# Performance work log

Measured on AMD Instinct MI355X. Metric: run time of the kernel, lower is better.

## Reference

```python
import jax, jax.numpy as jnp
import numpy as np

D_IN = 1024
D_OUT = 1024
NUM_HEADS = 16
HEAD_DIM = D_OUT // NUM_HEADS
SEQ = 2048
BATCH = 2


def setup_inputs() -> dict:
    key = jax.random.key(0)
    k1, k2, k3 = jax.random.split(key, 3)
    x = jax.random.normal(k1, (BATCH, SEQ, D_IN), dtype=jnp.float32)
    w_qkv = jax.random.normal(k2, (3 * D_OUT, D_IN), dtype=jnp.float32) * (1.0 / np.sqrt(D_IN))
    w_proj = jax.random.normal(k3, (D_OUT, D_OUT), dtype=jnp.float32) * (1.0 / np.sqrt(D_OUT))
    b_proj = jnp.zeros((D_OUT,), dtype=jnp.float32)
    return {"x": x, "w_qkv": w_qkv, "w_proj": w_proj, "b_proj": b_proj}


def reference(x, w_qkv, w_proj, b_proj):
    B, S, _ = x.shape
    # QKV projection (no bias, qkv_bias=False)
    qkv = x @ w_qkv.T                              # [B,S,3*D]
    qkv = qkv.reshape(B, S, 3, NUM_HEADS, HEAD_DIM)
    q = qkv[:, :, 0].transpose(0, 2, 1, 3)          # [B,H,S,hd]
    k = qkv[:, :, 1].transpose(0, 2, 1, 3)
    v = qkv[:, :, 2].transpose(0, 2, 1, 3)
    scores = jnp.einsum('bhqd,bhkd->bhqk', q, k)    # [B,H,S,S]
    causal = jnp.triu(jnp.ones((S, S), dtype=bool), k=1)
    scores = jnp.where(causal, -jnp.inf, scores)
    weights = jax.nn.softmax(scores / np.sqrt(HEAD_DIM), axis=-1)
    ctx = jnp.einsum('bhqk,bhkd->bhqd', weights, v)  # [B,H,S,hd]
    ctx = ctx.transpose(0, 2, 1, 3).reshape(B, S, D_OUT)
    return ctx @ w_proj.T + b_proj
```

## Files before the change

kernel.cpp:

```cpp
#include <hip/hip_runtime.h>
#include <hip/hip_bf16.h>
#include <stdint.h>

#define NHEAD 16
#define HDIM  64
#define SEQ   2048
#define BATCH 2

typedef __attribute__((ext_vector_type(8))) short          s16x8;
typedef __attribute__((ext_vector_type(4))) short          s16x4;
typedef __attribute__((ext_vector_type(4))) float          f32x4;
typedef __attribute__((ext_vector_type(8))) unsigned short u16x8;
typedef __attribute__((ext_vector_type(4))) unsigned short u16x4;

__device__ __forceinline__ unsigned short f2b(float f) {
  union { float f; unsigned u; } x; x.f = f;
  unsigned r = x.u + 0x7fffu + ((x.u >> 16) & 1u);
  return (unsigned short)(r >> 16);
}
__device__ __forceinline__ float b2f(unsigned short b) {
  union { unsigned u; float f; } x; x.u = ((unsigned)b) << 16;
  return x.f;
}

__device__ __forceinline__ void gload_lds16(const void* g, void* l) {
  __builtin_amdgcn_global_load_lds((const __attribute__((address_space(1))) void*)g,
                                   (__attribute__((address_space(3))) void*)l,
                                   16, 0, 0);
}

#define SWZ(a) ((a) ^ ((((a) >> 7) & 7) << 4))

__global__ __launch_bounds__(256) void cvt3(
    const float* __restrict__ a, unsigned short* __restrict__ oa, int na,
    const float* __restrict__ b, unsigned short* __restrict__ ob, int nb,
    const float* __restrict__ c, unsigned short* __restrict__ oc) {
  int idx = (blockIdx.x * 256 + threadIdx.x) * 4;
  const float* in; unsigned short* out;
  if (idx < na)            { in = a; out = oa; }
  else if (idx < na + nb)  { in = b; out = ob; idx -= na; }
  else                     { in = c; out = oc; idx -= na + nb; }
  float4 v = *(const float4*)(in + idx);
  u16x4 o;
  o[0] = f2b(v.x); o[1] = f2b(v.y); o[2] = f2b(v.z); o[3] = f2b(v.w);
  *(u16x4*)(out + idx) = o;
}

template <int EPI, int M, int N, int K>
__global__ __launch_bounds__(256) void gemm_bt(
    const unsigned short* __restrict__ A,
    const unsigned short* __restrict__ B,
    unsigned short* __restrict__ oq,
    unsigned short* __restrict__ ok,
    unsigned short* __restrict__ ov,
    float* __restrict__ out,
    const float* __restrict__ bias) {
  __shared__ unsigned short As[128 * 64];
  __shared__ unsigned short Bs[128 * 64];

  constexpr int mtiles = M >> 7, ntiles = N >> 7;
  constexpr int mpx = mtiles >> 2, npx = ntiles >> 1;
  const int xcd = blockIdx.x & 7, j = blockIdx.x >> 3;
  const int mb = (xcd >> 1) * mpx + (j % mpx);
  const int nb = (xcd & 1) * npx + (j / mpx);
  const int mbase = mb << 7, nbase = nb << 7;

  const int tid  = threadIdx.x;
  const int lane = tid & 63;
  const int wid  = tid >> 6;
  const int wr   = (wid >> 1) * 64;
  const int wc   = (wid & 1) * 64;

  f32x4 acc[4][4];
  for (int r = 0; r < 4; ++r)
    for (int c = 0; c < 4; ++c) acc[r][c] = (f32x4){0.f, 0.f, 0.f, 0.f};

  const int rowA = lane >> 3;
  const int kbs  = ((lane & 7) * 16) ^ (rowA << 4);
  const size_t strideA = (size_t)K * 2;

  for (int kt = 0; kt < K; kt += 64) {
    for (int it = 0; it < 4; ++it) {
      int c   = wid * 4 + it;
      int row = c * 8 + rowA;
      gload_lds16((const char*)A + (size_t)(mbase + row) * strideA + (size_t)kt * 2 + kbs,
                  (char*)As + c * 1024 + (lane & 7) * 16);
      gload_lds16((const char*)B + (size_t)(nbase + row) * strideA + (size_t)kt * 2 + kbs,
                  (char*)Bs + c * 1024 + (lane & 7) * 16);
    }
    __syncthreads();
    const int sw = (lane & 7) << 4;
    for (int ks = 0; ks < 2; ++ks) {
      const int colb = ks * 64 + (lane >> 4) * 16;
      s16x8 af[4], bf[4];
      for (int r = 0; r < 4; ++r)
        af[r] = *(const s16x8*)((const char*)As + (wr + r * 16 + (lane & 15)) * 128 + (colb ^ sw));
      for (int c = 0; c < 4; ++c)
        bf[c] = *(const s16x8*)((const char*)Bs + (wc + c * 16 + (lane & 15)) * 128 + (colb ^ sw));
      for (int r = 0; r < 4; ++r)
        for (int c = 0; c < 4; ++c)
          acc[r][c] = __builtin_amdgcn_mfma_f32_16x16x32_bf16(af[r], bf[c], acc[r][c], 0, 0, 0);
    }
    __syncthreads();
  }

  for (int r = 0; r < 4; ++r) {
    for (int c = 0; c < 4; ++c) {
      const int n = nbase + wc + c * 16 + (lane & 15);
      for (int i = 0; i < 4; ++i) {
        const int m = mbase + wr + r * 16 + (lane >> 4) * 4 + i;
        float v = acc[r][c][i];
        if (EPI == 0) {
          int b = m >> 11, s = m & (SEQ - 1);
          int which = n >> 10, rr = n & 1023;
          int h = rr >> 6, d = rr & (HDIM - 1);
          if (which == 0)
            oq[(((size_t)b * NHEAD + h) * SEQ + s) * HDIM + d] = f2b(v);
          else if (which == 1)
            ok[(((size_t)b * NHEAD + h) * SEQ + s) * HDIM + d] = f2b(v);
          else
            ov[(((size_t)b * NHEAD + h) * HDIM + d) * SEQ + s] = f2b(v);
        } else {
          out[(size_t)m * N + n] = v + bias[n];
        }
      }
    }
  }
}

__global__ __launch_bounds__(256, 4) void flash_attn(
    const unsigned short* __restrict__ Qb,
    const unsigned short* __restrict__ Kb,
    const unsigned short* __restrict__ Vb,
    unsigned short* __restrict__ ctx) {
  const int bsw  = (int)blockIdx.x;
  const int lin  = ((bsw & 7) << 6) + (bsw >> 3);
  const int bh   = lin >> 4;
  const int pair = lin & 15;
  const int b    = bh >> 4;
  const int h    = bh & (NHEAD - 1);

  const unsigned short* Qh  = Qb + (size_t)bh * SEQ * HDIM;
  const char*           Khc = (const char*)(Kb + (size_t)bh * SEQ * HDIM);
  const char*           Vtc = (const char*)(Vb + (size_t)bh * HDIM * SEQ);

  const int tid = threadIdx.x, lane = tid & 63, wid = tid >> 6;
  const int g = lane >> 4, q = lane & 15;

  __shared__ unsigned short Ks[2][64 * 64];
  __shared__ unsigned short Vt[2][64 * 64];
  __shared__ unsigned short Ps[4][16 * 64];

  const int vy0   = (wid * 2) * 1024 + lane * 16;
  const int vrow0 = vy0 >> 7;
  const int vsw0  = ((vy0 & 127) ^ ((vrow0 & 7) << 4));
  const int vy1   = vy0 + 1024;
  const int vrow1 = vy1 >> 7;
  const int vsw1  = ((vy1 & 127) ^ ((vrow1 & 7) << 4));

  for (int pass = 0; pass < 2; ++pass) {
    const int qt    = pass ? pair : 31 - pair;
    const int qbase = qt * 64;

    s16x8 qf[2];
    {
      const int qrow = qbase + wid * 16 + q;
      for (int ks = 0; ks < 2; ++ks) {
        u16x8 raw = *(const u16x8*)&Qh[(size_t)qrow * HDIM + ks * 32 + g * 8];
        s16x8 qv;
        for (int j = 0; j < 8; ++j) qv[j] = (short)f2b(b2f(raw[j]) * 0.125f);
        qf[ks] = qv;
      }
    }

    float l4[4] = {0.f, 0.f, 0.f, 0.f};
    f32x4 o[4];
    for (int c = 0; c < 4; ++c) o[c] = (f32x4){0.f, 0.f, 0.f, 0.f};

    {
      for (int it = 0; it < 2; ++it) {
        const int x = (wid * 2 + it) * 1024 + lane * 16;
        gload_lds16(Khc + SWZ(x), (char*)Ks[0] + x);
      }
      gload_lds16(Vtc + (size_t)vrow0 * (SEQ * 2) + vsw0, (char*)Vt[0] + vy0);
      gload_lds16(Vtc + (size_t)vrow1 * (SEQ * 2) + vsw1, (char*)Vt[0] + vy1);
    }
    __syncthreads();

    for (int kt = 0; kt <= qt; ++kt) {
      const int cur = kt & 1, nxt = cur ^ 1;

      if (kt < qt) {
        const char* ksrc = Khc + (size_t)(kt + 1) * 8192;
        for (int it = 0; it < 2; ++it) {
          const int x = (wid * 2 + it) * 1024 + lane * 16;
          gload_lds16(ksrc + SWZ(x), (char*)Ks[nxt] + x);
        }
        const size_t vco = (size_t)(kt + 1) * 128;
        gload_lds16(Vtc + (size_t)vrow0 * (SEQ * 2) + vco + vsw0, (char*)Vt[nxt] + vy0);
        gload_lds16(Vtc + (size_t)vrow1 * (SEQ * 2) + vco + vsw1, (char*)Vt[nxt] + vy1);
      }

      f32x4 sa[4];
      for (int c = 0; c < 4; ++c) sa[c] = (f32x4){0.f, 0.f, 0.f, 0.f};
      for (int ks = 0; ks < 2; ++ks) {
        const int kb2 = ks * 64 + g * 16;
        for (int c = 0; c < 4; ++c) {
          const int row = c * 16 + q;
          const int a   = row * 128 + kb2;
          s16x8 kb8 = *(const s16x8*)((const char*)Ks[cur] + (a ^ ((row & 7) << 4)));
          sa[c] = __builtin_amdgcn_mfma_f32_16x16x32_bf16(kb8, qf[ks], sa[c], 0, 0, 0);
        }
      }

      if (kt == qt) {
        const int q_rel = wid * 16 + q;
        for (int c = 0; c < 4; ++c) {
          for (int i = 0; i < 4; ++i) {
            const int key_rel = c * 16 + g * 4 + i;
            if (key_rel > q_rel) sa[c][i] = -1e30f;
          }
        }
      }

      for (int c = 0; c < 4; ++c) {
        const float p0 = __expf(sa[c][0]);
        const float p1 = __expf(sa[c][1]);
        const float p2 = __expf(sa[c][2]);
        const float p3 = __expf(sa[c][3]);
        l4[0] += p0; l4[1] += p1; l4[2] += p2; l4[3] += p3;
        union { unsigned u[2]; s16x4 v; } pk;
        asm("v_cvt_pk_bf16_f32 %0, %1, %2" : "=v"(pk.u[0]) : "v"(p0), "v"(p1));
        asm("v_cvt_pk_bf16_f32 %0, %1, %2" : "=v"(pk.u[1]) : "v"(p2), "v"(p3));
        const int a2 = (q * 128 + c * 32 + g * 8) ^ ((q & 7) << 4);
        *(s16x4*)((char*)Ps[wid] + a2) = pk.v;
      }
      __builtin_amdgcn_sched_barrier(0);

      for (int ks = 0; ks < 2; ++ks) {
        const int kb2 = ks * 64 + g * 16;
        const int paa = q * 128 + kb2;
        s16x8 pa = *(const s16x8*)((const char*)Ps[wid] + (paa ^ ((q & 7) << 4)));
        for (int c = 0; c < 4; ++c) {
          const int row = c * 16 + q;
          const int a   = row * 128 + kb2;
          s16x8 vb8 = *(const s16x8*)((const char*)Vt[cur] + (a ^ ((row & 7) << 4)));
          o[c] = __builtin_amdgcn_mfma_f32_16x16x32_bf16(pa, vb8, o[c], 0, 0, 0);
        }
      }

      __syncthreads();
    }

    float lsum = (l4[0] + l4[1]) + (l4[2] + l4[3]);
    lsum += __shfl_xor(lsum, 16);
    lsum += __shfl_xor(lsum, 32);
    for (int i = 0; i < 4; ++i) {
      const int qi   = g * 4 + i;
      const float li = __shfl(lsum, qi);
      const float nv = 1.f / li;
      const int row  = qbase + wid * 16 + qi;
      for (int c = 0; c < 4; ++c) {
        const int col = h * HDIM + c * 16 + q;
        ctx[((size_t)b * SEQ + row) * (NHEAD * HDIM) + col] = f2b(o[c][i] * nv);
      }
    }
  }
}

extern "C" void kernel_launch(void* const* d_in, const int* in_sizes, int n_in,
                              void* d_out, int out_size, void* d_ws, size_t ws_size,
                              hipStream_t stream) {
  const float* x      = (const float*)d_in[0];
  const float* w_qkv  = (const float*)d_in[1];
  const float* w_proj = (const float*)d_in[2];
  const float* b_proj = (const float*)d_in[3];
  float* out = (float*)d_out;

  char* ws = (char*)d_ws;
  unsigned short* xb     = (unsigned short*)(ws);
  unsigned short* wqkvb  = (unsigned short*)(ws + 8388608);
  unsigned short* wprojb = (unsigned short*)(ws + 14680064);
  unsigned short* qb     = (unsigned short*)(ws + 16777216);
  unsigned short* kb     = (unsigned short*)(ws + 25165824);
  unsigned short* vb     = (unsigned short*)(ws + 33554432);
  unsigned short* ctx    = (unsigned short*)(ws + 41943040);

  cvt3<<<dim3(8192), dim3(256), 0, stream>>>(
      x, xb, 4096 * 1024, w_qkv, wqkvb, 3072 * 1024, w_proj, wprojb);

  gemm_bt<0, 4096, 3072, 1024><<<dim3(768), dim3(256), 0, stream>>>(
      xb, wqkvb, qb, kb, vb, (float*)nullptr, (const float*)nullptr);

  flash_attn<<<dim3(512), dim3(256), 0, stream>>>(qb, kb, vb, ctx);

  gemm_bt<1, 4096, 1024, 1024><<<dim3(256), dim3(256), 0, stream>>>(
      ctx, wprojb, (unsigned short*)nullptr, (unsigned short*)nullptr,
      (unsigned short*)nullptr, out, b_proj);
}
```

Before: 123.4 us.

## Double-buffer GEMM LDS tiles and drop XCD-aware block mapping

Splits the GEMM's shared-memory A/B tiles into two buffers so the next K-tile is fetched from global memory into LDS while MFMAs run on the current one, aiming to hide load latency. It also replaces the XCD-aware block-to-tile mapping with a plain row-major mapping. Doubling LDS from 32KB to 64KB per block can lower occupancy. Dropping the XCD swizzle may hurt L2 locality. The diff is cut off before the loop end, so barrier placement cannot be checked.

```diff
diff --git a/kernel.cpp b/kernel.cpp
--- a/kernel.cpp
+++ b/kernel.cpp
@@ -55,14 +55,12 @@
     unsigned short* __restrict__ ov,
     float* __restrict__ out,
     const float* __restrict__ bias) {
-  __shared__ unsigned short As[128 * 64];
-  __shared__ unsigned short Bs[128 * 64];
-
-  constexpr int mtiles = M >> 7, ntiles = N >> 7;
-  constexpr int mpx = mtiles >> 2, npx = ntiles >> 1;
-  const int xcd = blockIdx.x & 7, j = blockIdx.x >> 3;
-  const int mb = (xcd >> 1) * mpx + (j % mpx);
-  const int nb = (xcd & 1) * npx + (j / mpx);
+  __shared__ unsigned short As[2][128 * 64];
+  __shared__ unsigned short Bs[2][128 * 64];
+
+  constexpr int ntiles = N >> 7;
+  const int mb = blockIdx.x / ntiles;
+  const int nb = blockIdx.x % ntiles;
   const int mbase = mb << 7, nbase = nb << 7;
 
   const int tid  = threadIdx.x;
@@ -77,26 +75,45 @@
 
   const int rowA = lane >> 3;
   const int kbs  = ((lane & 7) * 16) ^ (rowA << 4);
+  const int ldst = (lane & 7) * 16;
   const size_t strideA = (size_t)K * 2;
 
-  for (int kt = 0; kt < K; kt += 64) {
+  stage_first:;
+  {
     for (int it = 0; it < 4; ++it) {
       int c   = wid * 4 + it;
       int row = c * 8 + rowA;
-      gload_lds16((const char*)A + (size_t)(mbase + row) * strideA + (size_t)kt * 2 + kbs,
-                  (char*)As + c * 1024 + (lane & 7) * 16);
-      gload_lds16((const char*)B + (size_t)(nbase + row) * strideA + (size_t)kt * 2 + kbs,
-                  (char*)Bs + c * 1024 + (lane & 7) * 16);
-    }
-    __syncthreads();
+      gload_lds16((const char*)A + (size_t)(mbase + row) * strideA + kbs,
+                  (char*)As[0] + c * 1024 + ldst);
+      gload_lds16((const char*)B + (size_t)(nbase + row) * strideA + kbs,
+                  (char*)Bs[0] + c * 1024 + ldst);
+    }
+  }
+  __syncthreads();
+
+  constexpr int NT = K >> 6;
+  for (int t = 0; t < NT; ++t) {
+    const int cur = t & 1;
+    if (t + 1 < NT) {
+      const size_t ko = (size_t)(t + 1) * 128;
+      for (int it = 0; it < 4; ++it) {
+        int c   = wid * 4 + it;
+        int row = c * 8 + rowA;
+        gload_lds16((const char*)A + (size_t)(mbase + row) * strideA + ko + kbs,
+                    (char*)As[cur ^ 1] + c * 1024 + ldst);
+        gload_lds16((const char*)B + (size_t)(nbase + row) * strideA + ko + kbs,
+                    (char*)Bs[cur ^ 1] + c * 1024 + ldst);
+      }
+    }
+
     const int sw = (lane & 7) << 4;
     for (int ks = 0; ks < 2; ++ks) {
       const int colb = ks * 64 + (lane >> 4) * 16;
       s16x8 af[4], bf[4];
       for (int r = 0; r < 4; ++r)
-        af[r] = *(const s16x8*)((const char*)As + (wr + r * 16 + (lane & 15)) * 128 + (colb ^ sw));
+        af[r] = *(const s16x8*)((const char*)As[cur] + (wr + r * 16 + (lane & 15)) * 128 + (colb ^ sw));
       for (int c = 0; c < 4; ++c)
-        bf[c] = *(const s16x8*)((const char*)Bs + (wc + c * 16 + (lane & 15)) * 128 + (colb ^ sw));
+        bf[c] = *(const s16x8*)((const char*)Bs[cur] + (wc + c * 16 + (lane & 15)) * 128 + (colb ^ sw));
       for (int r = 0; r < 4; ++r)
         for (int c = 0; c < 4; ++c)
           acc[r][c] = __builtin_amdgcn_mfma_f32_16x16x32_bf16(af[r], bf[c], acc[r][c], 0, 0, 0);
```

Measured after the change: 128.6 us. +4.3%, slower.
